# Optimization experiments

Hardware: AMD Instinct MI355X
Metric: run time of the kernel (lower is better)

Reference implementation:

```python
import jax, jax.numpy as jnp
import numpy as np

N_NODES = 100000
N_EDGES = 1600000
IN_DIM = 128
HID_DIM = 64
OUT_DIM = 64


def setup_inputs() -> dict:
    key = jax.random.key(0)
    ks = jax.random.split(key, 8)
    x = jax.random.normal(ks[0], (N_NODES, IN_DIM), dtype=jnp.float32)
    edge_index = jax.random.randint(ks[1], (2, N_EDGES), 0, N_NODES, dtype=jnp.int64)
    edge_weight = jax.random.uniform(ks[2], (N_EDGES,), dtype=jnp.float32)  # cached PPMI values
    # Glorot-style params for the two PPMIConv layers
    W1 = jax.random.normal(ks[3], (IN_DIM, HID_DIM), dtype=jnp.float32) * (1.0 / np.sqrt(IN_DIM))
    b1 = jnp.zeros((HID_DIM,), dtype=jnp.float32)
    W2 = jax.random.normal(ks[4], (HID_DIM, OUT_DIM), dtype=jnp.float32) * (1.0 / np.sqrt(HID_DIM))
    b2 = jnp.zeros((OUT_DIM,), dtype=jnp.float32)
    return {"x": x, "edge_index": edge_index, "edge_weight": edge_weight,
            "W1": W1, "b1": b1, "W2": W2, "b2": b2}


def _gcn_norm(edge_index, edge_weight, num_nodes):
    # symmetric normalization of (PPMI) edge weights: D^{-1/2} A D^{-1/2}
    row, col = edge_index[0], edge_index[1]
    deg = jax.ops.segment_sum(edge_weight, row, num_segments=num_nodes)
    deg_inv_sqrt = jnp.where(deg > 0, jax.lax.rsqrt(jnp.maximum(deg, 1e-12)), 0.0)
    return deg_inv_sqrt[row] * edge_weight * deg_inv_sqrt[col]


def _ppmi_conv(x, W, b, edge_index, norm, num_nodes):
    h = x @ W                                   # [N, D_out] transform
    msg = h[edge_index[0]] * norm[:, None]      # [E, D_out] gather + weight
    out = jax.ops.segment_sum(msg, edge_index[1], num_segments=num_nodes)  # scatter-add
    return out + b


def reference(x, edge_index, edge_weight, W1, b1, W2, b2):
    n = x.shape[0]
    norm = _gcn_norm(edge_index, edge_weight, n)
    h = _ppmi_conv(x, W1, b1, edge_index, norm, n)
    h = jax.nn.relu(h)
    h = _ppmi_conv(h, W2, b2, edge_index, norm, n)
    return h
```

## Files before the change

kernel.cpp:

```cpp
#include <hip/hip_runtime.h>
#include <hip/hip_fp16.h>

#define N_NODES 100000
#define N_EDGES 1600000
#define IN_DIM 128
#define HID_DIM 64
#define OUT_DIM 64
#define NBKT 196
#define BSH 9
#define BMSK 511
#define NBLK 500
#define CHUNK 3200
#define MROW (NBKT * NBLK)

typedef _Float16 half8 __attribute__((ext_vector_type(8)));
typedef float f32x4 __attribute__((ext_vector_type(4)));

__global__ void count_kernel(const int* __restrict__ rows, const int* __restrict__ cols,
                             int* __restrict__ M,
                             const float* __restrict__ W1, const float* __restrict__ W2,
                             __half* __restrict__ F1, __half* __restrict__ F2) {
    __shared__ unsigned hc[NBKT], hr[NBKT];
    if (blockIdx.x >= NBLK) {
        int t = (blockIdx.x - NBLK) * 256 + threadIdx.x;
        if (t < 1024) {
            int lane = t & 63, fg = t >> 6;
            int col = (fg & 3) * 16 + (lane & 15);
            int kb = (fg >> 2) * 32 + (lane >> 4) * 8;
            __half v[8];
#pragma unroll
            for (int j = 0; j < 8; ++j) v[j] = __float2half(W1[(kb + j) * 64 + col]);
            *reinterpret_cast<uint4*>(F1 + (size_t)t * 8) = *reinterpret_cast<uint4*>(v);
        } else if (t < 1536) {
            int u = t - 1024;
            int lane = u & 63, fg = u >> 6;
            int col = (fg & 3) * 16 + (lane & 15);
            int kb = (fg >> 2) * 32 + (lane >> 4) * 8;
            __half v[8];
#pragma unroll
            for (int j = 0; j < 8; ++j) v[j] = __float2half(W2[(kb + j) * 64 + col]);
            *reinterpret_cast<uint4*>(F2 + (size_t)u * 8) = *reinterpret_cast<uint4*>(v);
        }
        return;
    }
    for (int i = threadIdx.x; i < NBKT; i += 256) { hc[i] = 0; hr[i] = 0; }
    __syncthreads();
    const int4* r4 = (const int4*)(rows + blockIdx.x * CHUNK);
    const int4* c4 = (const int4*)(cols + blockIdx.x * CHUNK);
    for (int i = threadIdx.x; i < CHUNK / 4; i += 256) {
        int4 r = r4[i], c = c4[i];
        atomicAdd(&hr[r.x >> BSH], 1u); atomicAdd(&hr[r.y >> BSH], 1u);
        atomicAdd(&hr[r.z >> BSH], 1u); atomicAdd(&hr[r.w >> BSH], 1u);
        atomicAdd(&hc[c.x >> BSH], 1u); atomicAdd(&hc[c.y >> BSH], 1u);
        atomicAdd(&hc[c.z >> BSH], 1u); atomicAdd(&hc[c.w >> BSH], 1u);
    }
    __syncthreads();
    for (int i = threadIdx.x; i < NBKT; i += 256) {
        M[i * NBLK + blockIdx.x] = (int)hc[i];
        M[MROW + i * NBLK + blockIdx.x] = (int)hr[i];
    }
}

__global__ void block_sum_kernel(const int* __restrict__ counts, int* __restrict__ partials, int n) {
    __shared__ int sh[256];
    int base = blockIdx.x * 1024;
    int s = 0;
    for (int i = threadIdx.x; i < 1024; i += 256) {
        int idx = base + i;
        s += (idx < n) ? counts[idx] : 0;
    }
    sh[threadIdx.x] = s;
    __syncthreads();
    for (int off = 128; off > 0; off >>= 1) {
        if (threadIdx.x < off) sh[threadIdx.x] += sh[threadIdx.x + off];
        __syncthreads();
    }
    if (threadIdx.x == 0) partials[blockIdx.x] = sh[0];
}

__global__ void scan_partials_kernel(int* __restrict__ p, int nb) {
    __shared__ int sh[256];
    int t = threadIdx.x;
    int v = (t < nb) ? p[t] : 0;
    sh[t] = v;
    __syncthreads();
    for (int off = 1; off < 256; off <<= 1) {
        int add = (t >= off) ? sh[t - off] : 0;
        __syncthreads();
        sh[t] += add;
        __syncthreads();
    }
    if (t < nb) p[t] = sh[t] - v;
}

__global__ void scan_final_kernel(const int* __restrict__ counts, const int* __restrict__ partials,
                                  int* __restrict__ offsets, int n) {
    __shared__ int sh[256];
    int t = threadIdx.x;
    int idx0 = blockIdx.x * 1024 + t * 4;
    int v[4];
    int s = 0;
#pragma unroll
    for (int j = 0; j < 4; ++j) {
        int id = idx0 + j;
        v[j] = (id < n) ? counts[id] : 0;
        s += v[j];
    }
    sh[t] = s;
    __syncthreads();
    for (int off = 1; off < 256; off <<= 1) {
        int add = (t >= off) ? sh[t - off] : 0;
        __syncthreads();
        sh[t] += add;
        __syncthreads();
    }
    int run = sh[t] - s + partials[blockIdx.x];
#pragma unroll
    for (int j = 0; j < 4; ++j) {
        int id = idx0 + j;
        if (id < n) offsets[id] = run;
        run += v[j];
    }
    if (idx0 <= n - 1 && n - 1 < idx0 + 4) offsets[n] = run;
}

__global__ __launch_bounds__(256) void scatter_kernel(
        const int* __restrict__ rows, const int* __restrict__ cols,
        const float* __restrict__ w, const int* __restrict__ M, const int* __restrict__ Ms,
        unsigned long long* __restrict__ pkA, unsigned* __restrict__ pkR) {
    __shared__ unsigned long long pay[CHUNK];
    __shared__ unsigned char bkt[CHUNK];
    __shared__ unsigned scn[256];
    __shared__ unsigned base[NBKT], cur[NBKT], gbase[NBKT];
    const int blk = blockIdx.x, t = threadIdx.x;
    const int s = blk * CHUNK;
    const int4* r4 = (const int4*)(rows + s);
    const int4* c4 = (const int4*)(cols + s);
    const float4* w4 = (const float4*)(w + s);

    unsigned cnt = (t < NBKT) ? (unsigned)M[t * NBLK + blk] : 0;
    scn[t] = cnt;
    __syncthreads();
    for (int off = 1; off < 256; off <<= 1) {
        unsigned a = (t >= off) ? scn[t - off] : 0;
        __syncthreads();
        scn[t] += a;
        __syncthreads();
    }
    if (t < NBKT) {
        unsigned b0 = scn[t] - cnt;
        base[t] = b0; cur[t] = b0;
        gbase[t] = (unsigned)Ms[t * NBLK + blk];
    }
    __syncthreads();
#define PUTA(RV, CV, WV) { unsigned b = (unsigned)(CV) >> BSH; \
        unsigned p = atomicAdd(&cur[b], 1u); \
        pay[p] = ((unsigned long long)__float_as_uint(WV) << 32) | \
                 (unsigned)((((CV) & BMSK) << 17) | (RV)); \
        bkt[p] = (unsigned char)b; }
    for (int i = t; i < CHUNK / 4; i += 256) {
        int4 rr = r4[i]; int4 cc = c4[i]; float4 ww = w4[i];
        PUTA(rr.x, cc.x, ww.x); PUTA(rr.y, cc.y, ww.y);
        PUTA(rr.z, cc.z, ww.z); PUTA(rr.w, cc.w, ww.w);
    }
    __syncthreads();
    for (int i = t; i < CHUNK; i += 256) {
        unsigned b = bkt[i];
        pkA[gbase[b] + (i - base[b])] = pay[i];
    }
    __syncthreads();

    cnt = (t < NBKT) ? (unsigned)M[MROW + t * NBLK + blk] : 0;
    scn[t] = cnt;
    __syncthreads();
    for (int off = 1; off < 256; off <<= 1) {
        unsigned a = (t >= off) ? scn[t - off] : 0;
        __syncthreads();
        scn[t] += a;
        __syncthreads();
    }
    if (t < NBKT) {
        unsigned b0 = scn[t] - cnt;
        base[t] = b0; cur[t] = b0;
        gbase[t] = (unsigned)Ms[MROW + t * NBLK + blk] - (unsigned)N_EDGES;
    }
    __syncthreads();
    unsigned* pay32 = (unsigned*)pay;
#define PUTR(RV, WV) { unsigned b = (unsigned)(RV) >> BSH; \
        unsigned p = atomicAdd(&cur[b], 1u); \
        pay32[p] = ((unsigned)__half_as_ushort(__float2half(WV)) << 16) | (unsigned)((RV) & BMSK); \
        bkt[p] = (unsigned char)b; }
    for (int i = t; i < CHUNK / 4; i += 256) {
        int4 rr = r4[i]; float4 ww = w4[i];
        PUTR(rr.x, ww.x); PUTR(rr.y, ww.y); PUTR(rr.z, ww.z); PUTR(rr.w, ww.w);
    }
    __syncthreads();
    for (int i = t; i < CHUNK; i += 256) {
        unsigned b = bkt[i];
        pkR[gbase[b] + (i - base[b])] = pay32[i];
    }
}

__global__ __launch_bounds__(256) void fill_deg_kernel(
        const unsigned long long* __restrict__ pkA, const unsigned* __restrict__ pkR,
        const int* __restrict__ Ms, int2* __restrict__ csr,
        int* __restrict__ offsets, float* __restrict__ dis) {
    __shared__ unsigned sh[768];
    const int t = threadIdx.x;
    if (blockIdx.x < NBKT) {
        unsigned* hist = sh;
        unsigned* pairs = sh + 512;
        const int b = blockIdx.x;
        hist[t] = 0; hist[t + 256] = 0;
        __syncthreads();
        const int s = Ms[b * NBLK];
        const int e = Ms[(b + 1) * NBLK];
        for (int i = s + t; i < e; i += 256) {
            unsigned lo = (unsigned)pkA[i];
            atomicAdd(&hist[(lo >> 17) & (unsigned)BMSK], 1u);
        }
        __syncthreads();
        unsigned h0 = hist[2 * t], h1 = hist[2 * t + 1];
        pairs[t] = h0 + h1;
        __syncthreads();
        for (int off = 1; off < 256; off <<= 1) {
            unsigned add = (t >= off) ? pairs[t - off] : 0;
            __syncthreads();
            pairs[t] += add;
            __syncthreads();
        }
        unsigned P = pairs[t] - (h0 + h1) + (unsigned)s;
        unsigned e0 = P, e1 = P + h0;
        int n0 = b * 512 + 2 * t;
        int n1 = n0 + 1;
        if (n0 <= N_NODES) offsets[n0] = (int)e0;
        if (n1 <= N_NODES) offsets[n1] = (int)e1;
        hist[2 * t] = e0; hist[2 * t + 1] = e1;
        __syncthreads();
        for (int i = s + t; i < e; i += 256) {
            unsigned long long p = pkA[i];
            unsigned lo = (unsigned)p;
            unsigned cl = (lo >> 17) & (unsigned)BMSK;
            int r = (int)(lo & 0x1FFFFu);
            unsigned pos = atomicAdd(&hist[cl], 1u);
            csr[pos] = make_int2(r, (int)(unsigned)(p >> 32));
        }
    } else {
        float* acc = (float*)sh;
        const int b = blockIdx.x - NBKT;
        acc[t] = 0.f; acc[t + 256] = 0.f;
        __syncthreads();
        const int s = Ms[MROW + b * NBLK] - N_EDGES;
        const int e = Ms[MROW + (b + 1) * NBLK] - N_EDGES;
        for (int i = s + t; i < e; i += 256) {
            unsigned u = pkR[i];
            float wv = __half2float(__ushort_as_half((unsigned short)(u >> 16)));
            atomicAdd(&acc[u & (unsigned)BMSK], wv);
        }
        __syncthreads();
#pragma unroll
        for (int k = 0; k < 2; ++k) {
            int node = b * 512 + t + k * 256;
            if (node < N_NODES) {
                float d = acc[t + k * 256];
                dis[node] = d > 0.f ? rsqrtf(fmaxf(d, 1e-12f)) : 0.f;
            }
        }
    }
}

__global__ __launch_bounds__(256) void gemm1_mfma(
        const float* __restrict__ x, const __half* __restrict__ F1,
        const float* __restrict__ dis, __half* __restrict__ h1) {
    const int wid = threadIdx.x >> 6, lane = threadIdx.x & 63;
    const int row0 = blockIdx.x * 64 + wid * 16;
    int arow = min(row0 + (lane & 15), N_NODES - 1);
    const int kb0 = (lane >> 4) * 8;
    const float* ap = x + (size_t)arow * 128 + kb0;

    f32x4 acc[4] = {};
#pragma unroll
    for (int c = 0; c < 4; ++c) {
        float4 a0 = *reinterpret_cast<const float4*>(ap + c * 32);
        float4 a1 = *reinterpret_cast<const float4*>(ap + c * 32 + 4);
        half8 af;
        af[0] = (_Float16)a0.x; af[1] = (_Float16)a0.y; af[2] = (_Float16)a0.z; af[3] = (_Float16)a0.w;
        af[4] = (_Float16)a1.x; af[5] = (_Float16)a1.y; af[6] = (_Float16)a1.z; af[7] = (_Float16)a1.w;
#pragma unroll
        for (int ct = 0; ct < 4; ++ct) {
            half8 bf = *reinterpret_cast<const half8*>(F1 + ((size_t)(c * 4 + ct) * 64 + lane) * 8);
            acc[ct] = __builtin_amdgcn_mfma_f32_16x16x32_f16(af, bf, acc[ct], 0, 0, 0);
        }
    }
    const int prow = row0 + ((lane >> 4) << 2);
    const int col = lane & 15;
#pragma unroll
    for (int r = 0; r < 4; ++r) {
        int rr = prow + r;
        if (rr < N_NODES) {
            float dv = dis[rr];
#pragma unroll
            for (int ct = 0; ct < 4; ++ct)
                h1[(size_t)rr * 64 + ct * 16 + col] = __float2half(acc[ct][r] * dv);
        }
    }
}

__global__ __launch_bounds__(256) void gemm2_mfma(
        const __half* __restrict__ g, const __half* __restrict__ F2,
        const float* __restrict__ b2, float* __restrict__ out) {
    const int wid = threadIdx.x >> 6, lane = threadIdx.x & 63;
    const int row0 = blockIdx.x * 64 + wid * 16;
    int arow = min(row0 + (lane & 15), N_NODES - 1);
    const int kb0 = (lane >> 4) * 8;
    const __half* ap = g + (size_t)arow * 64 + kb0;

    f32x4 acc[4] = {};
#pragma unroll
    for (int c = 0; c < 2; ++c) {
        half8 af = *reinterpret_cast<const half8*>(ap + c * 32);
#pragma unroll
        for (int ct = 0; ct < 4; ++ct) {
            half8 bf = *reinterpret_cast<const half8*>(F2 + ((size_t)(c * 4 + ct) * 64 + lane) * 8);
            acc[ct] = __builtin_amdgcn_mfma_f32_16x16x32_f16(af, bf, acc[ct], 0, 0, 0);
        }
    }
    const int prow = row0 + ((lane >> 4) << 2);
    const int col = lane & 15;
#pragma unroll
    for (int ct = 0; ct < 4; ++ct) {
        float bb = b2[ct * 16 + col];
#pragma unroll
        for (int r = 0; r < 4; ++r) {
            int rr = prow + r;
            if (rr < N_NODES) out[(size_t)rr * 64 + ct * 16 + col] = acc[ct][r] + bb;
        }
    }
}

__device__ __forceinline__ void fma8(float* a, uint4 u, float nv) {
    float2 f;
    f = __half22float2(__builtin_bit_cast(__half2, u.x)); a[0] = fmaf(f.x, nv, a[0]); a[1] = fmaf(f.y, nv, a[1]);
    f = __half22float2(__builtin_bit_cast(__half2, u.y)); a[2] = fmaf(f.x, nv, a[2]); a[3] = fmaf(f.y, nv, a[3]);
    f = __half22float2(__builtin_bit_cast(__half2, u.z)); a[4] = fmaf(f.x, nv, a[4]); a[5] = fmaf(f.y, nv, a[5]);
    f = __half22float2(__builtin_bit_cast(__half2, u.w)); a[6] = fmaf(f.x, nv, a[6]); a[7] = fmaf(f.y, nv, a[7]);
}

template <int BIAS_RELU>
__device__ __forceinline__ void gather_epilogue(float* a, int node, int q,
                                                const float* bias, const float* dis,
                                                __half* outh) {
    float dv = dis[node];
    if (BIAS_RELU) {
        const float4 b0 = *reinterpret_cast<const float4*>(bias + (q << 3));
        const float4 b1 = *reinterpret_cast<const float4*>(bias + (q << 3) + 4);
        a[0] = fmaxf(fmaf(a[0], dv, b0.x), 0.f) * dv; a[1] = fmaxf(fmaf(a[1], dv, b0.y), 0.f) * dv;
        a[2] = fmaxf(fmaf(a[2], dv, b0.z), 0.f) * dv; a[3] = fmaxf(fmaf(a[3], dv, b0.w), 0.f) * dv;
        a[4] = fmaxf(fmaf(a[4], dv, b1.x), 0.f) * dv; a[5] = fmaxf(fmaf(a[5], dv, b1.y), 0.f) * dv;
        a[6] = fmaxf(fmaf(a[6], dv, b1.z), 0.f) * dv; a[7] = fmaxf(fmaf(a[7], dv, b1.w), 0.f) * dv;
    } else {
#pragma unroll
        for (int k = 0; k < 8; ++k) a[k] *= dv;
    }
    __half2 o0 = __float22half2_rn(make_float2(a[0], a[1]));
    __half2 o1 = __float22half2_rn(make_float2(a[2], a[3]));
    __half2 o2 = __float22half2_rn(make_float2(a[4], a[5]));
    __half2 o3 = __float22half2_rn(make_float2(a[6], a[7]));
    uint4 u = make_uint4(__builtin_bit_cast(unsigned, o0), __builtin_bit_cast(unsigned, o1),
                         __builtin_bit_cast(unsigned, o2), __builtin_bit_cast(unsigned, o3));
    *reinterpret_cast<uint4*>(outh + ((size_t)node << 6) + (q << 3)) = u;
}

template <int BIAS_RELU>
__global__ __launch_bounds__(512) void gather_vec_kernel(
        const __half* __restrict__ h, const int2* __restrict__ csr,
        const int* __restrict__ offsets, const float* __restrict__ bias,
        const float* __restrict__ dis, __half* __restrict__ outh, int n) {
    const int wid = threadIdx.x >> 6;
    const int n0 = blockIdx.x * 16 + wid * 2;
    const int n1 = n0 + 1;
    const int lane = threadIdx.x & 63;
    const int q = lane & 7;
    const int g = lane >> 3;
    const int s0 = offsets[n0], e0 = offsets[n0 + 1];
    const int s1 = offsets[n1], e1 = offsets[n1 + 1];
    const int cl0 = max(e0 - 1, s0);
    const int cl1 = max(e1 - 1, s1);

    float xa[8] = {}, ya[8] = {};
    const int L = max(e0 - s0, e1 - s1);
    for (int j = 0; j < L; j += 16) {
        int iA0 = s0 + j + g,     iB0 = s0 + j + 8 + g;
        int iA1 = s1 + j + g,     iB1 = s1 + j + 8 + g;
        int2 pA0 = csr[min(iA0, cl0)];
        int2 pB0 = csr[min(iB0, cl0)];
        int2 pA1 = csr[min(iA1, cl1)];
        int2 pB1 = csr[min(iB1, cl1)];
        uint4 uA0 = *reinterpret_cast<const uint4*>(h + ((size_t)pA0.x << 6) + (q << 3));
        uint4 uB0 = *reinterpret_cast<const uint4*>(h + ((size_t)pB0.x << 6) + (q << 3));
        uint4 uA1 = *reinterpret_cast<const uint4*>(h + ((size_t)pA1.x << 6) + (q << 3));
        uint4 uB1 = *reinterpret_cast<const uint4*>(h + ((size_t)pB1.x << 6) + (q << 3));
        float nA0 = (iA0 < e0) ? __int_as_float(pA0.y) : 0.f;
        float nB0 = (iB0 < e0) ? __int_as_float(pB0.y) : 0.f;
        float nA1 = (iA1 < e1) ? __int_as_float(pA1.y) : 0.f;
        float nB1 = (iB1 < e1) ? __int_as_float(pB1.y) : 0.f;
        fma8(xa, uA0, nA0); fma8(xa, uB0, nB0);
        fma8(ya, uA1, nA1); fma8(ya, uB1, nB1);
    }
#pragma unroll
    for (int m = 8; m <= 32; m <<= 1) {
#pragma unroll
        for (int k = 0; k < 8; ++k) {
            xa[k] += __shfl_xor(xa[k], m);
            ya[k] += __shfl_xor(ya[k], m);
        }
    }
    if (g == 0) {
        gather_epilogue<BIAS_RELU>(xa, n0, q, bias, dis, outh);
    } else if (g == 1) {
        gather_epilogue<BIAS_RELU>(ya, n1, q, bias, dis, outh);
    }
}

extern "C" void kernel_launch(void* const* d_in, const int* in_sizes, int n_in,
                              void* d_out, int out_size, void* d_ws, size_t ws_size,
                              hipStream_t stream) {
    const float* x  = (const float*)d_in[0];
    const int*   ei = (const int*)d_in[1];
    const float* ew = (const float*)d_in[2];
    const float* W1 = (const float*)d_in[3];
    const float* b1 = (const float*)d_in[4];
    const float* W2 = (const float*)d_in[5];
    const float* b2 = (const float*)d_in[6];
    float* out = (float*)d_out;
    char*  ws  = (char*)d_ws;

    const int* rows = ei;
    const int* cols = ei + N_EDGES;

    int2*     csr      = (int2*)(ws + 0);
    unsigned long long* pkA = (unsigned long long*)(ws + 12800000);
    unsigned* pkR      = (unsigned*)(ws + 25600000);
    __half*   h1       = (__half*)(ws + 12800000);
    __half*   g        = (__half*)(ws + 12800000);
    __half*   t        = (__half*)(ws + 25600000);
    int*      M        = (int*)(ws + 38400000);
    int*      Ms       = (int*)(ws + 39184000);
    int*      partials = (int*)(ws + 39968016);
    int*      offsets  = (int*)(ws + 39968784);
    float*    dis      = (float*)(ws + 40368800);
    __half*   F1       = (__half*)(ws + 40768800);
    __half*   F2       = (__half*)(ws + 40785184);

    const int TPB = 256;
    const int n2  = 2 * MROW;
    const int nSB2 = (n2 + 1023) / 1024;

    count_kernel<<<NBLK + 6, TPB, 0, stream>>>(rows, cols, M, W1, W2, F1, F2);

    block_sum_kernel<<<nSB2, 256, 0, stream>>>(M, partials, n2);
    scan_partials_kernel<<<1, 256, 0, stream>>>(partials, nSB2);
    scan_final_kernel<<<nSB2, 256, 0, stream>>>(M, partials, Ms, n2);

    scatter_kernel<<<NBLK, TPB, 0, stream>>>(rows, cols, ew, M, Ms, pkA, pkR);

    fill_deg_kernel<<<2 * NBKT, TPB, 0, stream>>>(pkA, pkR, Ms, csr, offsets, dis);

    gemm1_mfma<<<(N_NODES + 63) / 64, TPB, 0, stream>>>(x, F1, dis, h1);

    gather_vec_kernel<1><<<N_NODES / 16, 512, 0, stream>>>(h1, csr, offsets, b1, dis, t, N_NODES);

    gather_vec_kernel<0><<<N_NODES / 16, 512, 0, stream>>>(t, csr, offsets, b1, dis, g, N_NODES);

    gemm2_mfma<<<(N_NODES + 63) / 64, TPB, 0, stream>>>(g, F2, b2, out);
}
```

Before: 164.1 us.

## Store hidden features in channel-sliced layout and gather per slice

Hidden feature matrices are stored as 8 slices of 8 channels each (a [slice][node][8] layout) instead of row-major [node][64]. The gather kernels now process one slice per block, so each slice's working set is smaller and more cache-resident, with 8 lanes per node striding over edges. The cost is that the CSR edge list is re-read 8 times per layer and the gemm1 stores become strided, with more, smaller blocks.

```diff
diff --git a/kernel.cpp b/kernel.cpp
--- a/kernel.cpp
+++ b/kernel.cpp
@@ -12,6 +12,7 @@
 #define NBLK 500
 #define CHUNK 3200
 #define MROW (NBKT * NBLK)
+#define SLICE_STRIDE ((size_t)N_NODES * 8)
 
 typedef _Float16 half8 __attribute__((ext_vector_type(8)));
 typedef float f32x4 __attribute__((ext_vector_type(4)));
@@ -300,8 +301,11 @@
         if (rr < N_NODES) {
             float dv = dis[rr];
 #pragma unroll
-            for (int ct = 0; ct < 4; ++ct)
-                h1[(size_t)rr * 64 + ct * 16 + col] = __float2half(acc[ct][r] * dv);
+            for (int ct = 0; ct < 4; ++ct) {
+                int ch = ct * 16 + col;
+                h1[(size_t)(ch >> 3) * SLICE_STRIDE + (size_t)rr * 8 + (ch & 7)] =
+                    __float2half(acc[ct][r] * dv);
+            }
         }
     }
 }
@@ -313,12 +317,12 @@
     const int row0 = blockIdx.x * 64 + wid * 16;
     int arow = min(row0 + (lane & 15), N_NODES - 1);
     const int kb0 = (lane >> 4) * 8;
-    const __half* ap = g + (size_t)arow * 64 + kb0;
 
     f32x4 acc[4] = {};
 #pragma unroll
     for (int c = 0; c < 2; ++c) {
-        half8 af = *reinterpret_cast<const half8*>(ap + c * 32);
+        int sl = (kb0 + c * 32) >> 3;
+        half8 af = *reinterpret_cast<const half8*>(g + (size_t)sl * SLICE_STRIDE + (size_t)arow * 8);
 #pragma unroll
         for (int ct = 0; ct < 4; ++ct) {
             half8 bf = *reinterpret_cast<const half8*>(F2 + ((size_t)(c * 4 + ct) * 64 + lane) * 8);
@@ -347,78 +351,51 @@
 }
 
 template <int BIAS_RELU>
-__device__ __forceinline__ void gather_epilogue(float* a, int node, int q,
-                                                const float* bias, const float* dis,
-                                                __half* outh) {
-    float dv = dis[node];
-    if (BIAS_RELU) {
-        const float4 b0 = *reinterpret_cast<const float4*>(bias + (q << 3));
-        const float4 b1 = *reinterpret_cast<const float4*>(bias + (q << 3) + 4);
-        a[0] = fmaxf(fmaf(a[0], dv, b0.x), 0.f) * dv; a[1] = fmaxf(fmaf(a[1], dv, b0.y), 0.f) * dv;
-        a[2] = fmaxf(fmaf(a[2], dv, b0.z), 0.f) * dv; a[3] = fmaxf(fmaf(a[3], dv, b0.w), 0.f) * dv;
-        a[4] = fmaxf(fmaf(a[4], dv, b1.x), 0.f) * dv; a[5] = fmaxf(fmaf(a[5], dv, b1.y), 0.f) * dv;
-        a[6] = fmaxf(fmaf(a[6], dv, b1.z), 0.f) * dv; a[7] = fmaxf(fmaf(a[7], dv, b1.w), 0.f) * dv;
-    } else {
-#pragma unroll
-        for (int k = 0; k < 8; ++k) a[k] *= dv;
-    }
-    __half2 o0 = __float22half2_rn(make_float2(a[0], a[1]));
-    __half2 o1 = __float22half2_rn(make_float2(a[2], a[3]));
-    __half2 o2 = __float22half2_rn(make_float2(a[4], a[5]));
-    __half2 o3 = __float22half2_rn(make_float2(a[6], a[7]));
-    uint4 u = make_uint4(__builtin_bit_cast(unsigned, o0), __builtin_bit_cast(unsigned, o1),
-                         __builtin_bit_cast(unsigned, o2), __builtin_bit_cast(unsigned, o3));
-    *reinterpret_cast<uint4*>(outh + ((size_t)node << 6) + (q << 3)) = u;
-}
-
-template <int BIAS_RELU>
-__global__ __launch_bounds__(512) void gather_vec_kernel(
-        const __half* __restrict__ h, const int2* __restrict__ csr,
+__global__ __launch_bounds__(512) void gather_slice_kernel(
+        const __half* __restrict__ hS, const int2* __restrict__ csr,
         const int* __restrict__ offsets, const float* __restrict__ bias,
-        const float* __restrict__ dis, __half* __restrict__ outh, int n) {
-    const int wid = threadIdx.x >> 6;
-    const int n0 = blockIdx.x * 16 + wid * 2;
-    const int n1 = n0 + 1;
+        const float* __restrict__ dis, __half* __restrict__ outS) {
+    const int s = blockIdx.x & 7;
+    const int chunk = blockIdx.x >> 3;
     const int lane = threadIdx.x & 63;
-    const int q = lane & 7;
-    const int g = lane >> 3;
-    const int s0 = offsets[n0], e0 = offsets[n0 + 1];
-    const int s1 = offsets[n1], e1 = offsets[n1 + 1];
-    const int cl0 = max(e0 - 1, s0);
-    const int cl1 = max(e1 - 1, s1);
-
-    float xa[8] = {}, ya[8] = {};
-    const int L = max(e0 - s0, e1 - s1);
-    for (int j = 0; j < L; j += 16) {
-        int iA0 = s0 + j + g,     iB0 = s0 + j + 8 + g;
-        int iA1 = s1 + j + g,     iB1 = s1 + j + 8 + g;
-        int2 pA0 = csr[min(iA0, cl0)];
-        int2 pB0 = csr[min(iB0, cl0)];
-        int2 pA1 = csr[min(iA1, cl1)];
-        int2 pB1 = csr[min(iB1, cl1)];
-        uint4 uA0 = *reinterpret_cast<const uint4*>(h + ((size_t)pA0.x << 6) + (q << 3));
-        uint4 uB0 = *reinterpret_cast<const uint4*>(h + ((size_t)pB0.x << 6) + (q << 3));
-        uint4 uA1 = *reinterpret_cast<const uint4*>(h + ((size_t)pA1.x << 6) + (q << 3));
-        uint4 uB1 = *reinterpret_cast<const uint4*>(h + ((size_t)pB1.x << 6) + (q << 3));
-        float nA0 = (iA0 < e0) ? __int_as_float(pA0.y) : 0.f;
-        float nB0 = (iB0 < e0) ? __int_as_float(pB0.y) : 0.f;
-        float nA1 = (iA1 < e1) ? __int_as_float(pA1.y) : 0.f;
-        float nB1 = (iB1 < e1) ? __int_as_float(pB1.y) : 0.f;
-        fma8(xa, uA0, nA0); fma8(xa, uB0, nB0);
-        fma8(ya, uA1, nA1); fma8(ya, uB1, nB1);
-    }
-#pragma unroll
-    for (int m = 8; m <= 32; m <<= 1) {
-#pragma unroll
-        for (int k = 0; k < 8; ++k) {
-            xa[k] += __shfl_xor(xa[k], m);
-            ya[k] += __shfl_xor(ya[k], m);
-        }
-    }
-    if (g == 0) {
-        gather_epilogue<BIAS_RELU>(xa, n0, q, bias, dis, outh);
-    } else if (g == 1) {
-        gather_epilogue<BIAS_RELU>(ya, n1, q, bias, dis, outh);
+    const int eslot = lane & 7;
+    const int node = chunk * 64 + (threadIdx.x >> 6) * 8 + (lane >> 3);
+    const __half* hp = hS + (size_t)s * SLICE_STRIDE;
+
+    int sn = 0, en = 0;
+    if (node < N_NODES) { sn = offsets[node]; en = offsets[node + 1]; }
+
+    float a[8] = {};
+    for (int j = sn + eslot; j < en; j += 8) {
+        int2 p = csr[j];
+        uint4 u = *reinterpret_cast<const uint4*>(hp + (size_t)p.x * 8);
+        fma8(a, u, __int_as_float(p.y));
+    }
+#pragma unroll
+    for (int m = 1; m <= 4; m <<= 1)
+#pragma unroll
+        for (int k = 0; k < 8; ++k) a[k] += __shfl_xor(a[k], m);
+
+    if (eslot == 0 && node < N_NODES) {
+        float dv = dis[node];
+        if (BIAS_RELU) {
+            const float4 b0 = *reinterpret_cast<const float4*>(bias + s * 8);
+            const float4 b1 = *reinterpret_cast<const float4*>(bias + s * 8 + 4);
+            a[0] = fmaxf(fmaf(a[0], dv, b0.x), 0.f) * dv; a[1] = fmaxf(fmaf(a[1], dv, b0.y), 0.f) * dv;
+            a[2] = fmaxf(fmaf(a[2], dv, b0.z), 0.f) * dv; a[3] = fmaxf(fmaf(a[3], dv, b0.w), 0.f) * dv;
+            a[4] = fmaxf(fmaf(a[4], dv, b1.x), 0.f) * dv; a[5] = fmaxf(fmaf(a[5], dv, b1.y), 0.f) * dv;
+            a[6] = fmaxf(fmaf(a[6], dv, b1.z), 0.f) * dv; a[7] = fmaxf(fmaf(a[7], dv, b1.w), 0.f) * dv;
+        } else {
+#pragma unroll
+            for (int k = 0; k < 8; ++k) a[k] *= dv;
+        }
+        __half2 o0 = __float22half2_rn(make_float2(a[0], a[1]));
+        __half2 o1 = __float22half2_rn(make_float2(a[2], a[3]));
+        __half2 o2 = __float22half2_rn(make_float2(a[4], a[5]));
+        __half2 o3 = __float22half2_rn(make_float2(a[6], a[7]));
+        uint4 u = make_uint4(__builtin_bit_cast(unsigned, o0), __builtin_bit_cast(unsigned, o1),
+                             __builtin_bit_cast(unsigned, o2), __builtin_bit_cast(unsigned, o3));
+        *reinterpret_cast<uint4*>(outS + (size_t)s * SLICE_STRIDE + (size_t)node * 8) = u;
     }
 }
 
@@ -455,6 +432,7 @@
     const int TPB = 256;
     const int n2  = 2 * MROW;
     const int nSB2 = (n2 + 1023) / 1024;
+    const int nChunks = (N_NODES + 63) / 64;
 
     count_kernel<<<NBLK + 6, TPB, 0, stream>>>(rows, cols, M, W1, W2, F1, F2);
 
@@ -468,9 +446,9 @@
 
     gemm1_mfma<<<(N_NODES + 63) / 64, TPB, 0, stream>>>(x, F1, dis, h1);
 
-    gather_vec_kernel<1><<<N_NODES / 16, 512, 0, stream>>>(h1, csr, offsets, b1, dis, t, N_NODES);
-
-    gather_vec_kernel<0><<<N_NODES / 16, 512, 0, stream>>>(t, csr, offsets, b1, dis, g, N_NODES);
+    gather_slice_kernel<1><<<nChunks * 8, 512, 0, stream>>>(h1, csr, offsets, b1, dis, t);
+
+    gather_slice_kernel<0><<<nChunks * 8, 512, 0, stream>>>(t, csr, offsets, b1, dis, g);
 
     gemm2_mfma<<<(N_NODES + 63) / 64, TPB, 0, stream>>>(g, F2, b2, out);
 }
```

Measured after the change: 224.2 us. 1.37x slower.

## Fuse second gather with output GEMM and use nontemporal CSR loads

Applied to the files above, without the earlier changes.

Merges the layer-2 gather and the final 64x64 MFMA GEMM into one kernel. Each block stages its 16 aggregated rows in shared memory and four waves compute the output tiles, which removes the intermediate g buffer write/read and one kernel launch. CSR loads and the gather1 output stores now use nontemporal hints to reduce cache pollution of the gathered feature table. The cost is a block-wide barrier and half the waves sitting idle during the GEMM step, and the nontemporal store on t may hurt because gather2 re-reads t randomly.

```diff
diff --git a/kernel.cpp b/kernel.cpp
--- a/kernel.cpp
+++ b/kernel.cpp
@@ -15,6 +15,17 @@
 
 typedef _Float16 half8 __attribute__((ext_vector_type(8)));
 typedef float f32x4 __attribute__((ext_vector_type(4)));
+typedef unsigned uint4v __attribute__((ext_vector_type(4)));
+typedef unsigned long long u64;
+
+__device__ __forceinline__ int2 ldnt_i2(const int2* p) {
+    u64 v = __builtin_nontemporal_load((const u64*)p);
+    return make_int2((int)(unsigned)v, (int)(v >> 32));
+}
+__device__ __forceinline__ void stnt_u4(void* p, uint4 v) {
+    uint4v t = {v.x, v.y, v.z, v.w};
+    __builtin_nontemporal_store(t, (uint4v*)p);
+}
 
 __global__ void count_kernel(const int* __restrict__ rows, const int* __restrict__ cols,
                              int* __restrict__ M,
@@ -306,38 +317,6 @@
     }
 }
 
-__global__ __launch_bounds__(256) void gemm2_mfma(
-        const __half* __restrict__ g, const __half* __restrict__ F2,
-        const float* __restrict__ b2, float* __restrict__ out) {
-    const int wid = threadIdx.x >> 6, lane = threadIdx.x & 63;
-    const int row0 = blockIdx.x * 64 + wid * 16;
-    int arow = min(row0 + (lane & 15), N_NODES - 1);
-    const int kb0 = (lane >> 4) * 8;
-    const __half* ap = g + (size_t)arow * 64 + kb0;
-
-    f32x4 acc[4] = {};
-#pragma unroll
-    for (int c = 0; c < 2; ++c) {
-        half8 af = *reinterpret_cast<const half8*>(ap + c * 32);
-#pragma unroll
-        for (int ct = 0; ct < 4; ++ct) {
-            half8 bf = *reinterpret_cast<const half8*>(F2 + ((size_t)(c * 4 + ct) * 64 + lane) * 8);
-            acc[ct] = __builtin_amdgcn_mfma_f32_16x16x32_f16(af, bf, acc[ct], 0, 0, 0);
-        }
-    }
-    const int prow = row0 + ((lane >> 4) << 2);
-    const int col = lane & 15;
-#pragma unroll
-    for (int ct = 0; ct < 4; ++ct) {
-        float bb = b2[ct * 16 + col];
-#pragma unroll
-        for (int r = 0; r < 4; ++r) {
-            int rr = prow + r;
-            if (rr < N_NODES) out[(size_t)rr * 64 + ct * 16 + col] = acc[ct][r] + bb;
-        }
-    }
-}
-
 __device__ __forceinline__ void fma8(float* a, uint4 u, float nv) {
     float2 f;
     f = __half22float2(__builtin_bit_cast(__half2, u.x)); a[0] = fmaf(f.x, nv, a[0]); a[1] = fmaf(f.y, nv, a[1]);
@@ -346,56 +325,22 @@
     f = __half22float2(__builtin_bit_cast(__half2, u.w)); a[6] = fmaf(f.x, nv, a[6]); a[7] = fmaf(f.y, nv, a[7]);
 }
 
-template <int BIAS_RELU>
-__device__ __forceinline__ void gather_epilogue(float* a, int node, int q,
-                                                const float* bias, const float* dis,
-                                                __half* outh) {
-    float dv = dis[node];
-    if (BIAS_RELU) {
-        const float4 b0 = *reinterpret_cast<const float4*>(bias + (q << 3));
-        const float4 b1 = *reinterpret_cast<const float4*>(bias + (q << 3) + 4);
-        a[0] = fmaxf(fmaf(a[0], dv, b0.x), 0.f) * dv; a[1] = fmaxf(fmaf(a[1], dv, b0.y), 0.f) * dv;
-        a[2] = fmaxf(fmaf(a[2], dv, b0.z), 0.f) * dv; a[3] = fmaxf(fmaf(a[3], dv, b0.w), 0.f) * dv;
-        a[4] = fmaxf(fmaf(a[4], dv, b1.x), 0.f) * dv; a[5] = fmaxf(fmaf(a[5], dv, b1.y), 0.f) * dv;
-        a[6] = fmaxf(fmaf(a[6], dv, b1.z), 0.f) * dv; a[7] = fmaxf(fmaf(a[7], dv, b1.w), 0.f) * dv;
-    } else {
-#pragma unroll
-        for (int k = 0; k < 8; ++k) a[k] *= dv;
-    }
-    __half2 o0 = __float22half2_rn(make_float2(a[0], a[1]));
-    __half2 o1 = __float22half2_rn(make_float2(a[2], a[3]));
-    __half2 o2 = __float22half2_rn(make_float2(a[4], a[5]));
-    __half2 o3 = __float22half2_rn(make_float2(a[6], a[7]));
-    uint4 u = make_uint4(__builtin_bit_cast(unsigned, o0), __builtin_bit_cast(unsigned, o1),
-                         __builtin_bit_cast(unsigned, o2), __builtin_bit_cast(unsigned, o3));
-    *reinterpret_cast<uint4*>(outh + ((size_t)node << 6) + (q << 3)) = u;
-}
-
-template <int BIAS_RELU>
-__global__ __launch_bounds__(512) void gather_vec_kernel(
+__device__ __forceinline__ void gather_pair(
         const __half* __restrict__ h, const int2* __restrict__ csr,
-        const int* __restrict__ offsets, const float* __restrict__ bias,
-        const float* __restrict__ dis, __half* __restrict__ outh, int n) {
-    const int wid = threadIdx.x >> 6;
-    const int n0 = blockIdx.x * 16 + wid * 2;
-    const int n1 = n0 + 1;
-    const int lane = threadIdx.x & 63;
-    const int q = lane & 7;
-    const int g = lane >> 3;
+        const int* __restrict__ offsets, int n0, int n1, int q, int g,
+        float* xa, float* ya) {
     const int s0 = offsets[n0], e0 = offsets[n0 + 1];
     const int s1 = offsets[n1], e1 = offsets[n1 + 1];
     const int cl0 = max(e0 - 1, s0);
     const int cl1 = max(e1 - 1, s1);
-
-    float xa[8] = {}, ya[8] = {};
     const int L = max(e0 - s0, e1 - s1);
     for (int j = 0; j < L; j += 16) {
         int iA0 = s0 + j + g,     iB0 = s0 + j + 8 + g;
         int iA1 = s1 + j + g,     iB1 = s1 + j + 8 + g;
-        int2 pA0 = csr[min(iA0, cl0)];
-        int2 pB0 = csr[min(iB0, cl0)];
-        int2 pA1 = csr[min(iA1, cl1)];
-        int2 pB1 = csr[min(iB1, cl1)];
+        int2 pA0 = ldnt_i2(&csr[min(iA0, cl0)]);
+        int2 pB0 = ldnt_i2(&csr[min(iB0, cl0)]);
+        int2 pA1 = ldnt_i2(&csr[min(iA1, cl1)]);
+        int2 pB1 = ldnt_i2(&csr[min(iB1, cl1)]);
         uint4 uA0 = *reinterpret_cast<const uint4*>(h + ((size_t)pA0.x << 6) + (q << 3));
         uint4 uB0 = *reinterpret_cast<const uint4*>(h + ((size_t)pB0.x << 6) + (q << 3));
         uint4 uA1 = *reinterpret_cast<const uint4*>(h + ((size_t)pA1.x << 6) + (q << 3));
@@ -415,10 +360,90 @@
             ya[k] += __shfl_xor(ya[k], m);
         }
     }
-    if (g == 0) {
-        gather_epilogue<BIAS_RELU>(xa, n0, q, bias, dis, outh);
-    } else if (g == 1) {
-        gather_epilogue<BIAS_RELU>(ya, n1, q, bias, dis, outh);
+}
+
+__global__ __launch_bounds__(512) void gather1_kernel(
+        const __half* __restrict__ h, const int2* __restrict__ csr,
+        const int* __restrict__ offsets, const float* __restrict__ bias,
+        const float* __restrict__ dis, __half* __restrict__ outh) {
+    const int wid = threadIdx.x >> 6;
+    const int n0 = blockIdx.x * 16 + wid * 2;
+    const int n1 = n0 + 1;
+    const int lane = threadIdx.x & 63;
+    const int q = lane & 7;
+    const int g = lane >> 3;
+
+    float xa[8] = {}, ya[8] = {};
+    gather_pair(h, csr, offsets, n0, n1, q, g, xa, ya);
+
+    if (g <= 1) {
+        float* a = (g == 0) ? xa : ya;
+        int node = (g == 0) ? n0 : n1;
+        float dv = dis[node];
+        const float4 b0 = *reinterpret_cast<const float4*>(bias + (q << 3));
+        const float4 b1 = *reinterpret_cast<const float4*>(bias + (q << 3) + 4);
+        a[0] = fmaxf(fmaf(a[0], dv, b0.x), 0.f) * dv; a[1] = fmaxf(fmaf(a[1], dv, b0.y), 0.f) * dv;
+        a[2] = fmaxf(fmaf(a[2], dv, b0.z), 0.f) * dv; a[3] = fmaxf(fmaf(a[3], dv, b0.w), 0.f) * dv;
+        a[4] = fmaxf(fmaf(a[4], dv, b1.x), 0.f) * dv; a[5] = fmaxf(fmaf(a[5], dv, b1.y), 0.f) * dv;
+        a[6] = fmaxf(fmaf(a[6], dv, b1.z), 0.f) * dv; a[7] = fmaxf(fmaf(a[7], dv, b1.w), 0.f) * dv;
+        __half2 o0 = __float22half2_rn(make_float2(a[0], a[1]));
+        __half2 o1 = __float22half2_rn(make_float2(a[2], a[3]));
+        __half2 o2 = __float22half2_rn(make_float2(a[4], a[5]));
+        __half2 o3 = __float22half2_rn(make_float2(a[6], a[7]));
+        uint4 u = make_uint4(__builtin_bit_cast(unsigned, o0), __builtin_bit_cast(unsigned, o1),
+                             __builtin_bit_cast(unsigned, o2), __builtin_bit_cast(unsigned, o3));
+        stnt_u4(outh + ((size_t)node << 6) + (q << 3), u);
+    }
+}
+
+__global__ __launch_bounds__(512) void gather2_gemm2_kernel(
+        const __half* __restrict__ h, const int2* __restrict__ csr,
+        const int* __restrict__ offsets, const float* __restrict__ dis,
+        const __half* __restrict__ F2, const float* __restrict__ b2,
+        float* __restrict__ out) {
+    __shared__ __half rows[16][72];
+    const int wid = threadIdx.x >> 6;
+    const int n0 = blockIdx.x * 16 + wid * 2;
+    const int n1 = n0 + 1;
+    const int lane = threadIdx.x & 63;
+    const int q = lane & 7;
+    const int g = lane >> 3;
+
+    float xa[8] = {}, ya[8] = {};
+    gather_pair(h, csr, offsets, n0, n1, q, g, xa, ya);
+
+    if (g <= 1) {
+        float* a = (g == 0) ? xa : ya;
+        int node = (g == 0) ? n0 : n1;
+        float dv = dis[node];
+#pragma unroll
+        for (int k = 0; k < 8; ++k) a[k] *= dv;
+        __half2 o0 = __float22half2_rn(make_float2(a[0], a[1]));
+        __half2 o1 = __float22half2_rn(make_float2(a[2], a[3]));
+        __half2 o2 = __float22half2_rn(make_float2(a[4], a[5]));
+        __half2 o3 = __float22half2_rn(make_float2(a[6], a[7]));
+        uint4 u = make_uint4(__builtin_bit_cast(unsigned, o0), __builtin_bit_cast(unsigned, o1),
+                             __builtin_bit_cast(unsigned, o2), __builtin_bit_cast(unsigned, o3));
+        *reinterpret_cast<uint4*>(&rows[wid * 2 + g][q << 3]) = u;
+    }
+    __syncthreads();
+
+    if (wid < 4) {
+        const int arow = lane & 15;
+        const int kb0 = (lane >> 4) * 8;
+        f32x4 acc = {};
+#pragma unroll
+        for (int c = 0; c < 2; ++c) {
+            half8 af = *reinterpret_cast<const half8*>(&rows[arow][c * 32 + kb0]);
+            half8 bf = *reinterpret_cast<const half8*>(F2 + ((size_t)(c * 4 + wid) * 64 + lane) * 8);
+            acc = __builtin_amdgcn_mfma_f32_16x16x32_f16(af, bf, acc, 0, 0, 0);
+        }
+        const int col = lane & 15;
+        const int prow = blockIdx.x * 16 + ((lane >> 4) << 2);
+        float bb = b2[wid * 16 + col];
+#pragma unroll
+        for (int r = 0; r < 4; ++r)
+            out[(size_t)(prow + r) * 64 + wid * 16 + col] = acc[r] + bb;
     }
 }
 
@@ -442,7 +467,6 @@
     unsigned long long* pkA = (unsigned long long*)(ws + 12800000);
     unsigned* pkR      = (unsigned*)(ws + 25600000);
     __half*   h1       = (__half*)(ws + 12800000);
-    __half*   g        = (__half*)(ws + 12800000);
     __half*   t        = (__half*)(ws + 25600000);
     int*      M        = (int*)(ws + 38400000);
     int*      Ms       = (int*)(ws + 39184000);
@@ -468,9 +492,7 @@
 
     gemm1_mfma<<<(N_NODES + 63) / 64, TPB, 0, stream>>>(x, F1, dis, h1);
 
-    gather_vec_kernel<1><<<N_NODES / 16, 512, 0, stream>>>(h1, csr, offsets, b1, dis, t, N_NODES);
-
-    gather_vec_kernel<0><<<N_NODES / 16, 512, 0, stream>>>(t, csr, offsets, b1, dis, g, N_NODES);
-
-    gemm2_mfma<<<(N_NODES + 63) / 64, TPB, 0, stream>>>(g, F2, b2, out);
-}
+    gather1_kernel<<<N_NODES / 16, 512, 0, stream>>>(h1, csr, offsets, b1, dis, t);
+
+    gather2_gemm2_kernel<<<N_NODES / 16, 512, 0, stream>>>(t, csr, offsets, dis, F2, b2, out);
+}
```

New measurement: 167.0 us. About the same (+1.8%).
